# Performance work log

Measured on AMD Instinct MI355X. Metric: run time of the kernel, lower is better.

The kernel has to match this reference:

```python
import jax, jax.numpy as jnp
import numpy as np

W, BHS, SEQ, H = 8, 2, 1024, 2048
FFN_PER = (4 * H) // W  # per-partition 4h width = 1024

def setup_inputs() -> dict:
    key = jax.random.key(0)
    k1, k2, k3 = jax.random.split(key, 3)
    # xavier-normal-ish scale for weights
    s1 = (2.0 / (H + FFN_PER)) ** 0.5
    s2 = (2.0 / (FFN_PER + H)) ** 0.5
    return {
        "hidden_states": jax.random.normal(k1, (W, BHS, SEQ, H), dtype=jnp.float32),
        "w1": jax.random.normal(k2, (W, H, FFN_PER), dtype=jnp.float32) * s1,
        "b1": jnp.zeros((W, 1, FFN_PER), dtype=jnp.float32),
        "w2": jax.random.normal(k3, (W, FFN_PER, H), dtype=jnp.float32) * s2,
        "b2": jnp.zeros((W, H), dtype=jnp.float32),
        "idx_list": jnp.arange(W, dtype=jnp.int64),
    }

def reference(hidden_states, w1, b1, w2, b2, idx_list):
    w, bhs, seq, h = hidden_states.shape
    # view [W, bhs, seq, h] -> [W, bhs*seq, h]
    x = hidden_states.reshape(w, bhs * seq, h)
    # column-parallel: baddbmm(bias, x, w1) -> [W, N, 4h/W]
    inter = jnp.einsum('wnh,whf->wnf', x, w1) + b1
    # exact (erf) gelu, matching torch F.gelu default
    inter = jax.nn.gelu(inter, approximate=False)
    # row-parallel: baddbmm(bias, inter, w2) -> [W, N, h]
    out_bias = b2[:, None, :]  # [W, 1, out]
    out = jnp.einsum('wnf,wfo->wno', inter, w2) + out_bias
    return (out, out_bias)
```

## Files before the change

### kernel.cpp

```cpp
#include <hip/hip_runtime.h>
#include <hip/hip_bf16.h>
#include <math.h>


typedef float f32x4 __attribute__((ext_vector_type(4)));
typedef short bf16x8 __attribute__((ext_vector_type(8)));
typedef short bf16x4 __attribute__((ext_vector_type(4)));
typedef unsigned short u16;

#define NW 8
#define MDIM 2048
#define HDIM 2048
#define FFN  1024

static __device__ __forceinline__ u16 f32_to_bf16_rn(float f) {
  union { float f; unsigned u; } v; v.f = f;
  unsigned r = v.u + 0x7FFF + ((v.u >> 16) & 1);
  return (u16)(r >> 16);
}

static __device__ __forceinline__ void gload_lds16(const void* g, void* l) {
  __builtin_amdgcn_global_load_lds(
      (const __attribute__((address_space(1))) void*)g,
      (__attribute__((address_space(3))) void*)l, 16, 0, 0);
}

static __device__ __forceinline__ void transpose_body(
    const float* __restrict__ in, u16* __restrict__ out, int R, int C,
    int bx, int by, int bz, u16 (*tile)[68]) {
  int w = bz;
  int c0 = bx * 64, r0 = by * 64;
  int t = threadIdx.x;
  const float* ip = in + (size_t)w * R * C;
  u16* op = out + (size_t)w * C * R;
  int tr = t >> 4;
  int tc4 = (t & 15) * 4;
#pragma unroll
  for (int j = 0; j < 4; ++j) {
    int r = tr + j * 16;
    f32x4 v = *(const f32x4*)(ip + (size_t)(r0 + r) * C + c0 + tc4);
    tile[r][tc4 + 0] = f32_to_bf16_rn(v.x);
    tile[r][tc4 + 1] = f32_to_bf16_rn(v.y);
    tile[r][tc4 + 2] = f32_to_bf16_rn(v.z);
    tile[r][tc4 + 3] = f32_to_bf16_rn(v.w);
  }
  __syncthreads();
#pragma unroll
  for (int j = 0; j < 4; ++j) {
    int c = tr + j * 16;
    bf16x4 p;
    p[0] = (short)tile[tc4 + 0][c];
    p[1] = (short)tile[tc4 + 1][c];
    p[2] = (short)tile[tc4 + 2][c];
    p[3] = (short)tile[tc4 + 3][c];
    *(bf16x4*)(op + (size_t)(c0 + c) * R + r0 + tc4) = p;
  }
}

#define NB_T1 4096
#define NB_T2 4096
#define NB_CV 32768

__global__ void prep_kernel(const float* __restrict__ hs,
                            const float* __restrict__ w1,
                            const float* __restrict__ w2,
                            const float* __restrict__ b2,
                            u16* __restrict__ Xb, u16* __restrict__ W1t,
                            u16* __restrict__ W2t, float* __restrict__ outb) {
  __shared__ u16 tile[64][68];
  int bid = blockIdx.x;
  if (bid < NB_T1) {
    transpose_body(w1, W1t, HDIM, FFN, bid % 16, (bid / 16) % 32, bid / 512,
                   tile);
    return;
  }
  bid -= NB_T1;
  if (bid < NB_T2) {
    transpose_body(w2, W2t, FFN, HDIM, bid % 32, (bid / 32) % 16, bid / 512,
                   tile);
    return;
  }
  bid -= NB_T2;
  if (bid < NB_CV) {
    size_t i = (size_t)bid * blockDim.x + threadIdx.x;
    f32x4 v = ((const f32x4*)hs)[i];
    bf16x4 p;
    p[0] = (short)f32_to_bf16_rn(v.x);
    p[1] = (short)f32_to_bf16_rn(v.y);
    p[2] = (short)f32_to_bf16_rn(v.z);
    p[3] = (short)f32_to_bf16_rn(v.w);
    ((bf16x4*)Xb)[i] = p;
    return;
  }
  bid -= NB_CV;
  {
    int i = bid * 256 + threadIdx.x;
    if (i < NW * HDIM) outb[i] = b2[i];
  }
}

#define STAGE_AH(dst, tt, h)                                                  \
  do {                                                                        \
    gload_lds16(gA + (size_t)(h) * 128 * rowK + (size_t)(tt) * 128,           \
                (dst) + (h) * 16384 + tid * 16);                              \
    gload_lds16(gA + ((size_t)(h) * 128 + 64) * rowK + (size_t)(tt) * 128,    \
                (dst) + (h) * 16384 + 8192 + tid * 16);                       \
  } while (0)
#define STAGE_BH(dst, tt, h)                                                  \
  do {                                                                        \
    gload_lds16(gB + (size_t)(h) * 128 * rowK + (size_t)(tt) * 128,           \
                (dst) + 32768 + (h) * 16384 + tid * 16);                      \
    gload_lds16(gB + ((size_t)(h) * 128 + 64) * rowK + (size_t)(tt) * 128,    \
                (dst) + 32768 + (h) * 16384 + 8192 + tid * 16);               \
  } while (0)

#define LOAD_A(DST, SB, q)                                                    \
  _Pragma("unroll") for (int ii = 0; ii < 2; ++ii)                            \
      _Pragma("unroll") for (int kk = 0; kk < 2; ++kk)                        \
          DST[ii][kk] = *(const bf16x8*)((SB) + Aoff +                        \
              ((q)*32 + ii * 16 + ra) * 128 + (colsw ^ (kk << 6)))
#define LOAD_B(DST, SB)                                                       \
  _Pragma("unroll") for (int jj = 0; jj < 4; ++jj)                            \
      _Pragma("unroll") for (int kk = 0; kk < 2; ++kk)                        \
          DST[jj][kk] = *(const bf16x8*)((SB) + Boff +                        \
              (brow + jj * 16 + ra) * 128 + (colsw ^ (kk << 6)))

#define MFMA_Q(q, AF)                                                         \
  {                                                                           \
    __builtin_amdgcn_s_setprio(1);                                            \
    _Pragma("unroll") for (int ii = 0; ii < 2; ++ii)                          \
        _Pragma("unroll") for (int jj = 0; jj < 4; ++jj)                      \
            _Pragma("unroll") for (int kk = 0; kk < 2; ++kk)                  \
                acc[(q)*2 + ii][jj] =                                         \
                    __builtin_amdgcn_mfma_f32_16x16x32_bf16(                  \
                        AF[ii][kk], bfr[jj][kk], acc[(q)*2 + ii][jj],         \
                        0, 0, 0);                                             \
    __builtin_amdgcn_s_setprio(0);                                            \
  }

template <bool GELU, bool C_F32>
__global__ __launch_bounds__(512, 2) void mlp_gemm(
    const u16* __restrict__ A, const u16* __restrict__ Bt,
    const float* __restrict__ bias, void* __restrict__ Cptr,
    int M, int N, int K, int nN) {
  __shared__ __align__(16) char lds[131072];
  char* cur = lds;
  char* nxt = lds + 65536;

  const int bid = blockIdx.x;
  const int w = bid & 7;
  const int jb = bid >> 3;
  const int m0 = (jb / nN) * 256;
  const int n0 = (jb % nN) * 256;

  const int tid = threadIdx.x;
  const int wid = tid >> 6, lane = tid & 63;
  const int wr = wid >> 2, wc = wid & 3;
  const int qa = lane >> 4, ra = lane & 15;

  const u16* ap = A + (size_t)w * M * K;
  const u16* btp = Bt + (size_t)w * N * K;
  const float* bp = bias + (size_t)w * N;

  const size_t rowK = (size_t)K * 2;
  const int r8 = tid >> 3;
  const int csw = ((tid & 7) * 16) ^ ((r8 & 7) << 4);
  const char* gA = (const char*)ap + (size_t)(m0 + r8) * rowK + csw;
  const char* gB = (const char*)btp + (size_t)(n0 + r8) * rowK + csw;

  const int colsw = (qa * 16) ^ ((ra & 7) << 4);
  const int Aoff = wr * 16384;
  const int Boff = 32768 + (wc >> 1) * 16384;
  const int brow = (wc & 1) * 64;

  f32x4 acc[8][4];
#pragma unroll
  for (int i = 0; i < 8; ++i)
#pragma unroll
    for (int j = 0; j < 4; ++j)
#pragma unroll
      for (int r = 0; r < 4; ++r) acc[i][j][r] = 0.0f;

  const int NT = K >> 6;

  STAGE_AH(cur, 0, 0); STAGE_AH(cur, 0, 1);
  STAGE_BH(cur, 0, 0); STAGE_BH(cur, 0, 1);
  asm volatile("s_waitcnt vmcnt(0)" ::: "memory");
  __builtin_amdgcn_s_barrier();
  __builtin_amdgcn_sched_barrier(0);

  bf16x8 bfr[4][2], afrA[2][2], afrB[2][2];
  LOAD_B(bfr, cur);
  LOAD_A(afrA, cur, 0);

  for (int t = 0; t < NT; ++t) {
    const bool pf = (t + 1) < NT;
    if (pf) {
      STAGE_AH(nxt, t + 1, 0); STAGE_AH(nxt, t + 1, 1);
      STAGE_BH(nxt, t + 1, 0); STAGE_BH(nxt, t + 1, 1);
    }
    __builtin_amdgcn_sched_barrier(0);

    LOAD_A(afrB, cur, 1);
    MFMA_Q(0, afrA);
    LOAD_A(afrA, cur, 2);
    MFMA_Q(1, afrB);
    LOAD_A(afrB, cur, 3);
    MFMA_Q(2, afrA);
    MFMA_Q(3, afrB);

    asm volatile("s_waitcnt vmcnt(0)" ::: "memory");
    __builtin_amdgcn_s_barrier();
    __builtin_amdgcn_sched_barrier(0);

    if (pf) {
      LOAD_B(bfr, nxt);
      LOAD_A(afrA, nxt, 0);
    }
    char* tp = cur; cur = nxt; nxt = tp;
  }

#pragma unroll
  for (int i = 0; i < 8; ++i) {
#pragma unroll
    for (int j = 0; j < 4; ++j) {
      int col = n0 + wc * 64 + j * 16 + ra;
      float bv = bp[col];
#pragma unroll
      for (int r = 0; r < 4; ++r) {
        int row = m0 + wr * 128 + i * 16 + qa * 4 + r;
        float v = acc[i][j][r] + bv;
        if (GELU) v = 0.5f * v * (1.0f + erff(v * 0.70710678118654752f));
        if (C_F32)
          ((float*)Cptr)[(size_t)w * M * N + (size_t)row * N + col] = v;
        else
          ((u16*)Cptr)[(size_t)w * M * N + (size_t)row * N + col] =
              f32_to_bf16_rn(v);
      }
    }
  }
}

extern "C" void kernel_launch(void* const* d_in, const int* in_sizes, int n_in,
                              void* d_out, int out_size, void* d_ws,
                              size_t ws_size, hipStream_t stream) {
  const float* hs = (const float*)d_in[0];
  const float* w1 = (const float*)d_in[1];
  const float* b1 = (const float*)d_in[2];
  const float* w2 = (const float*)d_in[3];
  const float* b2 = (const float*)d_in[4];

  u16* W1t = (u16*)d_ws;
  u16* W2t = W1t + (size_t)NW * FFN * HDIM;
  u16* inter = W2t + (size_t)NW * HDIM * FFN;
  u16* XbWs = inter + (size_t)NW * MDIM * FFN;
  size_t need = ((size_t)NW * FFN * HDIM * 2 + (size_t)NW * MDIM * FFN +
                 (size_t)NW * MDIM * HDIM) * sizeof(u16);
  u16* Xb = (ws_size >= need) ? XbWs : (u16*)d_out;

  float* outb = (float*)d_out + (size_t)NW * MDIM * HDIM;

  prep_kernel<<<dim3(NB_T1 + NB_T2 + NB_CV + 16), 256, 0, stream>>>(
      hs, w1, w2, b2, Xb, W1t, W2t, outb);

  mlp_gemm<true, false>
      <<<dim3(NW * (MDIM / 256) * (FFN / 256)), 512, 0, stream>>>(
          Xb, W1t, b1, inter, MDIM, FFN, HDIM, FFN / 256);
  mlp_gemm<false, true>
      <<<dim3(NW * (MDIM / 256) * (HDIM / 256)), 512, 0, stream>>>(
          inter, W2t, b2, d_out, MDIM, HDIM, FFN, HDIM / 256);
}
```

Before: 227.0 us.

## Shrink GEMM tiles to 128x256 with K=32 steps for higher occupancy

Retiles both MLP GEMMs from 256x256 output tiles with 64-wide K steps to 128x256 tiles with 32-wide K steps. LDS drops from 128KB to 48KB per block, the launch bound targets 4 blocks per CU, and the grid doubles. The LDS swizzle and the fragment loads are rewritten for the narrower 64-byte rows. The aim is more resident waves and better latency hiding, at the cost of less data reuse per tile, twice as many barriers per unit of K, and more global traffic for the B operand.

```diff
diff --git a/kernel.cpp b/kernel.cpp
--- a/kernel.cpp
+++ b/kernel.cpp
@@ -99,58 +99,47 @@
   }
 }
 
-#define STAGE_AH(dst, tt, h)                                                  \
+#define STAGE_T(dst, tt)                                                      \
   do {                                                                        \
-    gload_lds16(gA + (size_t)(h) * 128 * rowK + (size_t)(tt) * 128,           \
-                (dst) + (h) * 16384 + tid * 16);                              \
-    gload_lds16(gA + ((size_t)(h) * 128 + 64) * rowK + (size_t)(tt) * 128,    \
-                (dst) + (h) * 16384 + 8192 + tid * 16);                       \
+    gload_lds16(gA + (size_t)(tt) * 64, (dst) + tid * 16);                    \
+    gload_lds16(gB + (size_t)(tt) * 64, (dst) + 8192 + tid * 16);             \
+    gload_lds16(gB + (size_t)128 * rowK + (size_t)(tt) * 64,                  \
+                (dst) + 16384 + tid * 16);                                    \
   } while (0)
-#define STAGE_BH(dst, tt, h)                                                  \
-  do {                                                                        \
-    gload_lds16(gB + (size_t)(h) * 128 * rowK + (size_t)(tt) * 128,           \
-                (dst) + 32768 + (h) * 16384 + tid * 16);                      \
-    gload_lds16(gB + ((size_t)(h) * 128 + 64) * rowK + (size_t)(tt) * 128,    \
-                (dst) + 32768 + (h) * 16384 + 8192 + tid * 16);               \
-  } while (0)
-
-#define LOAD_A(DST, SB, q)                                                    \
+
+#define LOAD_A(DST, SB, h)                                                    \
   _Pragma("unroll") for (int ii = 0; ii < 2; ++ii)                            \
-      _Pragma("unroll") for (int kk = 0; kk < 2; ++kk)                        \
-          DST[ii][kk] = *(const bf16x8*)((SB) + Aoff +                        \
-              ((q)*32 + ii * 16 + ra) * 128 + (colsw ^ (kk << 6)))
+      DST[ii] = *(const bf16x8*)((SB) +                                       \
+          (wr * 64 + ((h)*2 + ii) * 16 + ra) * 64 + colsw)
 #define LOAD_B(DST, SB)                                                       \
   _Pragma("unroll") for (int jj = 0; jj < 4; ++jj)                            \
-      _Pragma("unroll") for (int kk = 0; kk < 2; ++kk)                        \
-          DST[jj][kk] = *(const bf16x8*)((SB) + Boff +                        \
-              (brow + jj * 16 + ra) * 128 + (colsw ^ (kk << 6)))
-
-#define MFMA_Q(q, AF)                                                         \
+      DST[jj] = *(const bf16x8*)((SB) + 8192 +                                \
+          (wc * 64 + jj * 16 + ra) * 64 + colsw)
+
+#define MFMA_H(h, AF)                                                         \
   {                                                                           \
     __builtin_amdgcn_s_setprio(1);                                            \
     _Pragma("unroll") for (int ii = 0; ii < 2; ++ii)                          \
         _Pragma("unroll") for (int jj = 0; jj < 4; ++jj)                      \
-            _Pragma("unroll") for (int kk = 0; kk < 2; ++kk)                  \
-                acc[(q)*2 + ii][jj] =                                         \
-                    __builtin_amdgcn_mfma_f32_16x16x32_bf16(                  \
-                        AF[ii][kk], bfr[jj][kk], acc[(q)*2 + ii][jj],         \
-                        0, 0, 0);                                             \
+            acc[(h)*2 + ii][jj] =                                             \
+                __builtin_amdgcn_mfma_f32_16x16x32_bf16(                      \
+                    AF[ii], bfr[jj], acc[(h)*2 + ii][jj], 0, 0, 0);           \
     __builtin_amdgcn_s_setprio(0);                                            \
   }
 
 template <bool GELU, bool C_F32>
-__global__ __launch_bounds__(512, 2) void mlp_gemm(
+__global__ __launch_bounds__(512, 4) void mlp_gemm(
     const u16* __restrict__ A, const u16* __restrict__ Bt,
     const float* __restrict__ bias, void* __restrict__ Cptr,
     int M, int N, int K, int nN) {
-  __shared__ __align__(16) char lds[131072];
+  __shared__ __align__(16) char lds[49152];
   char* cur = lds;
-  char* nxt = lds + 65536;
+  char* nxt = lds + 24576;
 
   const int bid = blockIdx.x;
   const int w = bid & 7;
   const int jb = bid >> 3;
-  const int m0 = (jb / nN) * 256;
+  const int m0 = (jb / nN) * 128;
   const int n0 = (jb % nN) * 256;
 
   const int tid = threadIdx.x;
@@ -163,51 +152,39 @@
   const float* bp = bias + (size_t)w * N;
 
   const size_t rowK = (size_t)K * 2;
-  const int r8 = tid >> 3;
-  const int csw = ((tid & 7) * 16) ^ ((r8 & 7) << 4);
-  const char* gA = (const char*)ap + (size_t)(m0 + r8) * rowK + csw;
-  const char* gB = (const char*)btp + (size_t)(n0 + r8) * rowK + csw;
-
-  const int colsw = (qa * 16) ^ ((ra & 7) << 4);
-  const int Aoff = wr * 16384;
-  const int Boff = 32768 + (wc >> 1) * 16384;
-  const int brow = (wc & 1) * 64;
-
-  f32x4 acc[8][4];
-#pragma unroll
-  for (int i = 0; i < 8; ++i)
+  const int csw = (((tid & 3) ^ ((tid >> 3) & 3)) * 16);
+  const char* gA = (const char*)ap + (size_t)(m0 + (tid >> 2)) * rowK + csw;
+  const char* gB = (const char*)btp + (size_t)(n0 + (tid >> 2)) * rowK + csw;
+
+  const int colsw = (qa * 16) ^ ((((ra >> 1) & 3)) << 4);
+
+  f32x4 acc[4][4];
+#pragma unroll
+  for (int i = 0; i < 4; ++i)
 #pragma unroll
     for (int j = 0; j < 4; ++j)
 #pragma unroll
       for (int r = 0; r < 4; ++r) acc[i][j][r] = 0.0f;
 
-  const int NT = K >> 6;
-
-  STAGE_AH(cur, 0, 0); STAGE_AH(cur, 0, 1);
-  STAGE_BH(cur, 0, 0); STAGE_BH(cur, 0, 1);
+  const int NT = K >> 5;
+
+  STAGE_T(cur, 0);
   asm volatile("s_waitcnt vmcnt(0)" ::: "memory");
   __builtin_amdgcn_s_barrier();
   __builtin_amdgcn_sched_barrier(0);
 
-  bf16x8 bfr[4][2], afrA[2][2], afrB[2][2];
+  bf16x8 bfr[4], afrA[2], afrB[2];
   LOAD_B(bfr, cur);
   LOAD_A(afrA, cur, 0);
 
   for (int t = 0; t < NT; ++t) {
     const bool pf = (t + 1) < NT;
-    if (pf) {
-      STAGE_AH(nxt, t + 1, 0); STAGE_AH(nxt, t + 1, 1);
-      STAGE_BH(nxt, t + 1, 0); STAGE_BH(nxt, t + 1, 1);
-    }
+    if (pf) STAGE_T(nxt, t + 1);
     __builtin_amdgcn_sched_barrier(0);
 
     LOAD_A(afrB, cur, 1);
-    MFMA_Q(0, afrA);
-    LOAD_A(afrA, cur, 2);
-    MFMA_Q(1, afrB);
-    LOAD_A(afrB, cur, 3);
-    MFMA_Q(2, afrA);
-    MFMA_Q(3, afrB);
+    MFMA_H(0, afrA);
+    MFMA_H(1, afrB);
 
     asm volatile("s_waitcnt vmcnt(0)" ::: "memory");
     __builtin_amdgcn_s_barrier();
@@ -221,14 +198,14 @@
   }
 
 #pragma unroll
-  for (int i = 0; i < 8; ++i) {
+  for (int i = 0; i < 4; ++i) {
 #pragma unroll
     for (int j = 0; j < 4; ++j) {
       int col = n0 + wc * 64 + j * 16 + ra;
       float bv = bp[col];
 #pragma unroll
       for (int r = 0; r < 4; ++r) {
-        int row = m0 + wr * 128 + i * 16 + qa * 4 + r;
+        int row = m0 + wr * 64 + i * 16 + qa * 4 + r;
         float v = acc[i][j][r] + bv;
         if (GELU) v = 0.5f * v * (1.0f + erff(v * 0.70710678118654752f));
         if (C_F32)
@@ -264,9 +241,9 @@
       hs, w1, w2, b2, Xb, W1t, W2t, outb);
 
   mlp_gemm<true, false>
-      <<<dim3(NW * (MDIM / 256) * (FFN / 256)), 512, 0, stream>>>(
+      <<<dim3(NW * (MDIM / 128) * (FFN / 256)), 512, 0, stream>>>(
           Xb, W1t, b1, inter, MDIM, FFN, HDIM, FFN / 256);
   mlp_gemm<false, true>
-      <<<dim3(NW * (MDIM / 256) * (HDIM / 256)), 512, 0, stream>>>(
+      <<<dim3(NW * (MDIM / 128) * (HDIM / 256)), 512, 0, stream>>>(
           inter, W2t, b2, d_out, MDIM, HDIM, FFN, HDIM / 256);
 }
```

Result: slower. 237.7 us (+4.7%).
